# Kernel tuning notes

Measured on AMD Instinct MI355X. Metric: run time of the kernel, lower is better.

## Reference

```python
import jax, jax.numpy as jnp
import numpy as np

B, T, HID, H, Dk, Dv, K = 2, 1024, 1024, 8, 128, 128, 4
EPS = 1e-5


def _dwconv_causal(y, w, b):
    # y: [B,T,C], w: [C,1,K], b: [C]; torch Conv1d(padding=K-1) then [:, :, :T] == causal left-pad
    C = y.shape[-1]
    z = jnp.transpose(y, (0, 2, 1))  # [B,C,T]
    z = jax.lax.conv_general_dilated(
        z, w, window_strides=(1,), padding=[(K - 1, 0)],
        feature_group_count=C, dimension_numbers=("NCH", "OIH", "NCH"))
    z = z + b[None, :, None]
    return jnp.transpose(z, (0, 2, 1))


def _forward(x, Wq, Wk, Wv, conv_q_w, conv_q_b, conv_k_w, conv_k_b,
             conv_v_w, conv_v_b, Wa, ba, Wb, bb, Wg, Wo, ln_g, ln_b):
    b_, t_ = x.shape[0], x.shape[1]
    q = jax.nn.silu(_dwconv_causal(x @ Wq, conv_q_w, conv_q_b))
    k = jax.nn.silu(_dwconv_causal(x @ Wk, conv_k_w, conv_k_b))
    v = jax.nn.silu(_dwconv_causal(x @ Wv, conv_v_w, conv_v_b))
    q = q.reshape(b_, t_, H, Dk)
    k = k.reshape(b_, t_, H, Dk) * (Dk ** -0.5)
    v = v.reshape(b_, t_, H, Dv)
    alpha = jax.nn.sigmoid(x @ Wa + ba)  # [B,T,H]
    beta = jax.nn.sigmoid(x @ Wb + bb)   # [B,T,H]

    # time-major for scan
    qt = jnp.transpose(q, (1, 0, 2, 3))  # [T,B,H,Dk]
    kt = jnp.transpose(k, (1, 0, 2, 3))
    vt = jnp.transpose(v, (1, 0, 2, 3))  # [T,B,H,Dv]
    at = jnp.transpose(alpha, (1, 0, 2))  # [T,B,H]
    bt = jnp.transpose(beta, (1, 0, 2))

    def step(S, inp):
        q_t, k_t, v_t, a_t, b_t = inp
        sk = jnp.einsum('bhij,bhj->bhi', S, k_t)          # S @ k
        err = sk - v_t                                     # [B,H,Dv]
        S = a_t[:, :, None, None] * S - b_t[:, :, None, None] * (err[..., None] * k_t[:, :, None, :])
        o_t = jnp.einsum('bhij,bhj->bhi', S, q_t)          # S @ q (post-update)
        return S, o_t

    S0 = jnp.zeros((b_, H, Dv, Dk), x.dtype)
    _, o = jax.lax.scan(step, S0, (qt, kt, vt, at, bt))
    o = jnp.transpose(o, (1, 0, 2, 3))  # [B,T,H,Dv]

    # LayerNorm over Dv
    mu = jnp.mean(o, axis=-1, keepdims=True)
    var = jnp.mean((o - mu) ** 2, axis=-1, keepdims=True)
    o = (o - mu) * jax.lax.rsqrt(var + EPS) * ln_g + ln_b

    g = jax.nn.sigmoid(x @ Wg).reshape(b_, t_, H, Dv)
    o = (o * g).reshape(b_, t_, H * Dv)
    return o @ Wo


def setup_inputs() -> dict:
    key = jax.random.key(0)
    ks = jax.random.split(key, 18)
    s = 0.02

    def n(k, shape, scale=s):
        return jax.random.normal(k, shape, jnp.float32) * scale

    return {
        "x": jax.random.normal(ks[0], (B, T, HID), jnp.float32),
        "Wq": n(ks[1], (HID, H * Dk)),
        "Wk": n(ks[2], (HID, H * Dk)),
        "Wv": n(ks[3], (HID, H * Dv)),
        "conv_q_w": n(ks[4], (H * Dk, 1, K), 0.25),
        "conv_q_b": n(ks[5], (H * Dk,), 0.1),
        "conv_k_w": n(ks[6], (H * Dk, 1, K), 0.25),
        "conv_k_b": n(ks[7], (H * Dk,), 0.1),
        "conv_v_w": n(ks[8], (H * Dv, 1, K), 0.25),
        "conv_v_b": n(ks[9], (H * Dv,), 0.1),
        "Wa": n(ks[10], (HID, H)),
        "ba": n(ks[11], (H,), 0.1),
        "Wb": n(ks[12], (HID, H)),
        "bb": n(ks[13], (H,), 0.1),
        "Wg": n(ks[14], (HID, H * Dv)),
        "Wo": n(ks[15], (H * Dv, HID)),
        "ln_g": jnp.ones((Dv,), jnp.float32),
        "ln_b": jnp.zeros((Dv,), jnp.float32),
    }


def reference(x, Wq, Wk, Wv, conv_q_w, conv_q_b, conv_k_w, conv_k_b,
              conv_v_w, conv_v_b, Wa, ba, Wb, bb, Wg, Wo, ln_g, ln_b):
    return _forward(x, Wq, Wk, Wv, conv_q_w, conv_q_b, conv_k_w, conv_k_b,
                    conv_v_w, conv_v_b, Wa, ba, Wb, bb, Wg, Wo, ln_g, ln_b)
```

## Files before the change

kernel.cpp:

```cpp
#include <hip/hip_runtime.h>

#define TSEQ 1024
#define HID_ 1024
#define NH 8
#define DK 128
#define DV 128
#define ROWS 2048
#define SZf (ROWS * HID_)
#define LCH 64
#define NCK 16
#define KSTR 136
#define ESTR 65

typedef __attribute__((ext_vector_type(8))) short short8;
typedef __attribute__((ext_vector_type(4))) float f32x4;
#define MFMA __builtin_amdgcn_mfma_f32_16x16x32_bf16

__device__ __forceinline__ float sig_(float x) { return 1.f / (1.f + __expf(-x)); }

__device__ __forceinline__ ushort f2bf(float f) {
    unsigned int u = __builtin_bit_cast(unsigned int, f);
    u += 0x7FFF + ((u >> 16) & 1);
    return (ushort)(u >> 16);
}
__device__ __forceinline__ float bf2f(ushort u) {
    return __builtin_bit_cast(float, ((unsigned int)u) << 16);
}
__device__ __forceinline__ unsigned int pk2(float lo, float hi) {
    return (unsigned int)f2bf(lo) | ((unsigned int)f2bf(hi) << 16);
}

__device__ __forceinline__ void gload16(const void* g, void* l) {
    __builtin_amdgcn_global_load_lds(
        (const __attribute__((address_space(1))) unsigned int*)g,
        (__attribute__((address_space(3))) unsigned int*)l, 16, 0, 0);
}

__global__ __launch_bounds__(256)
void k_x2bf(const float* __restrict__ x, ushort* __restrict__ xb)
{
    const size_t i8 = (size_t)blockIdx.x * 256 + threadIdx.x;
    float4 v0 = *(const float4*)(x + i8 * 8);
    float4 v1 = *(const float4*)(x + i8 * 8 + 4);
    uint4 o;
    o.x = pk2(v0.x, v0.y); o.y = pk2(v0.z, v0.w);
    o.z = pk2(v1.x, v1.y); o.w = pk2(v1.z, v1.w);
    *(uint4*)(xb + i8 * 8) = o;
}

__global__ __launch_bounds__(256)
void k_wT(const float* __restrict__ s0, const float* __restrict__ s1,
          const float* __restrict__ s2, const float* __restrict__ s3,
          ushort* __restrict__ dst)
{
    const int z = blockIdx.z;
    const float* W = (z == 0) ? s0 : (z == 1) ? s1 : (z == 2) ? s2 : s3;
    ushort* WT = dst + (size_t)z * (1024 * 1024);
    __shared__ float t[64][65];
    const int n0 = blockIdx.x * 64, k0 = blockIdx.y * 64;
    const int rr = threadIdx.x >> 4, cc = threadIdx.x & 15;
#pragma unroll
    for (int i = 0; i < 4; ++i) {
        const int row = i * 16 + rr;
        float4 v = *(const float4*)(W + (size_t)(k0 + row) * 1024 + n0 + cc * 4);
        t[row][cc * 4 + 0] = v.x; t[row][cc * 4 + 1] = v.y;
        t[row][cc * 4 + 2] = v.z; t[row][cc * 4 + 3] = v.w;
    }
    __syncthreads();
#pragma unroll
    for (int i = 0; i < 4; ++i) {
        const int n = i * 16 + rr;
        const int kc = cc * 4;
        ushort4 o;
        o.x = f2bf(t[kc + 0][n]); o.y = f2bf(t[kc + 1][n]);
        o.z = f2bf(t[kc + 2][n]); o.w = f2bf(t[kc + 3][n]);
        *(ushort4*)(WT + (size_t)(n0 + n) * 1024 + k0 + kc) = o;
    }
}

__device__ __forceinline__ void gemm_tile_mfma(const ushort* __restrict__ A,
                                               const ushort* __restrict__ BT,
                                               float* __restrict__ C,
                                               int brow, int bcol)
{
    __shared__ ushort As[128 * 64];
    __shared__ ushort Bs[128 * 64];
    const int tid  = threadIdx.x;
    const int lane = tid & 63;
    const int wv   = tid >> 6;
    const int wm   = (wv >> 1) * 64;
    const int wn   = (wv & 1) * 64;
    const int l15  = lane & 15;
    const int lq   = lane >> 4;

    f32x4 acc[4][4];
#pragma unroll
    for (int i = 0; i < 4; ++i)
#pragma unroll
        for (int j = 0; j < 4; ++j)
#pragma unroll
            for (int e = 0; e < 4; ++e) acc[i][j][e] = 0.f;

    for (int k0 = 0; k0 < 1024; k0 += 64) {
        __syncthreads();
#pragma unroll
        for (int j = 0; j < 4; ++j) {
            const int idx  = j * 256 + tid;
            const int row  = idx >> 3;
            const int gcol = ((idx & 7) ^ (row & 7)) * 8;
            const int ldst = (j * 256 + wv * 64) * 8;
            gload16(A  + (size_t)(brow + row) * 1024 + k0 + gcol, As + ldst);
            gload16(BT + (size_t)(bcol + row) * 1024 + k0 + gcol, Bs + ldst);
        }
        __syncthreads();
#pragma unroll
        for (int kk = 0; kk < 2; ++kk) {
            short8 af[4], bf[4];
#pragma unroll
            for (int i = 0; i < 4; ++i) {
                const int ra = wm + i * 16 + l15;
                af[i] = *(const short8*)(As + ra * 64 + (((kk * 4 + lq) ^ (ra & 7)) * 8));
            }
#pragma unroll
            for (int j = 0; j < 4; ++j) {
                const int rb = wn + j * 16 + l15;
                bf[j] = *(const short8*)(Bs + rb * 64 + (((kk * 4 + lq) ^ (rb & 7)) * 8));
            }
#pragma unroll
            for (int i = 0; i < 4; ++i)
#pragma unroll
                for (int j = 0; j < 4; ++j)
                    acc[i][j] = MFMA(af[i], bf[j], acc[i][j], 0, 0, 0);
        }
    }
    const int l4 = lane >> 4;
#pragma unroll
    for (int i = 0; i < 4; ++i)
#pragma unroll
        for (int j = 0; j < 4; ++j)
#pragma unroll
            for (int r = 0; r < 4; ++r)
                C[(size_t)(brow + wm + i * 16 + l4 * 4 + r) * 1024 +
                  bcol + wn + j * 16 + l15] = acc[i][j][r];
}

__global__ __launch_bounds__(256)
void k_gemm4(const ushort* __restrict__ A, const ushort* __restrict__ WT,
             float* __restrict__ Cbase)
{
    const ushort* BT = WT + (size_t)blockIdx.z * (1024 * 1024);
    float* C = Cbase + (size_t)blockIdx.z * SZf;
    gemm_tile_mfma(A, BT, C, blockIdx.y * 128, blockIdx.x * 128);
}

__global__ __launch_bounds__(256)
void k_gemm1(const ushort* __restrict__ A, const ushort* __restrict__ BT,
             float* __restrict__ C)
{
    gemm_tile_mfma(A, BT, C, blockIdx.y * 128, blockIdx.x * 128);
}

__global__ __launch_bounds__(256)
void k_ab(const float* __restrict__ x, const float* __restrict__ Wa,
          const float* __restrict__ ba, const float* __restrict__ Wb,
          const float* __restrict__ bb, float* __restrict__ aT,
          float* __restrict__ bT)
{
    const int r = blockIdx.x * 4 + (threadIdx.x >> 6);
    const int lane = threadIdx.x & 63;
    const int b = r >> 10, t = r & 1023;
    const float* xr = x + (size_t)r * HID_;
    float acc[16];
#pragma unroll
    for (int n = 0; n < 16; ++n) acc[n] = 0.f;
    for (int c = lane; c < HID_; c += 64) {
        const float xv = xr[c];
        const float* wa = Wa + c * 8;
        const float* wb = Wb + c * 8;
#pragma unroll
        for (int n = 0; n < 8; ++n) {
            acc[n]     = fmaf(xv, wa[n], acc[n]);
            acc[8 + n] = fmaf(xv, wb[n], acc[8 + n]);
        }
    }
#pragma unroll
    for (int n = 0; n < 16; ++n) {
#pragma unroll
        for (int m = 32; m; m >>= 1) acc[n] += __shfl_xor(acc[n], m);
    }
    if (lane < 8) {
        aT[(size_t)(b * 8 + lane) * TSEQ + t] = sig_(acc[lane] + ba[lane]);
        bT[(size_t)(b * 8 + lane) * TSEQ + t] = sig_(acc[8 + lane] + bb[lane]);
    }
}

__global__ __launch_bounds__(256)
void k_conv(const float* __restrict__ qf, const float* __restrict__ kf,
            const float* __restrict__ vf,
            const float* __restrict__ wq, const float* __restrict__ bq,
            const float* __restrict__ wk, const float* __restrict__ bk,
            const float* __restrict__ wv, const float* __restrict__ bv,
            ushort* __restrict__ Qst, ushort* __restrict__ Kst,
            ushort* __restrict__ Vrm)
{
    const int j = blockIdx.x >> 1, cg = blockIdx.x & 1;
    const int b = blockIdx.y, z = blockIdx.z;
    const float* src  = (z == 0) ? qf : (z == 1) ? kf : vf;
    const float* w    = (z == 0) ? wq : (z == 1) ? wk : wv;
    const float* bias = (z == 0) ? bq : (z == 1) ? bk : bv;
    const float scale = (z == 1) ? 0.08838834764831845f : 1.f;
    const int c2 = cg * 512 + threadIdx.x * 2;
    const float w0a = w[c2 * 4],     w1a = w[c2 * 4 + 1], w2a = w[c2 * 4 + 2], w3a = w[c2 * 4 + 3];
    const float w0b = w[c2 * 4 + 4], w1b = w[c2 * 4 + 5], w2b = w[c2 * 4 + 6], w3b = w[c2 * 4 + 7];
    const float bsa = bias[c2], bsb = bias[c2 + 1];
    float ya0 = 0.f, ya1 = 0.f, ya2 = 0.f, yb0 = 0.f, yb1 = 0.f, yb2 = 0.f;
    if (j > 0) {
#pragma unroll
        for (int i = 0; i < 3; ++i) {
            float2 t = *(const float2*)(src + (size_t)(b * TSEQ + j * 64 - 3 + i) * HID_ + c2);
            if (i == 0) { ya0 = t.x; yb0 = t.y; }
            else if (i == 1) { ya1 = t.x; yb1 = t.y; }
            else { ya2 = t.x; yb2 = t.y; }
        }
    }
    const int h = c2 >> 7, dk = c2 & 127;
    const int cid = (b * 8 + h) * 16 + j;
    ushort* dst = (z == 0) ? Qst : Kst;
#pragma unroll 4
    for (int tl = 0; tl < 64; ++tl) {
        float2 xv = *(const float2*)(src + (size_t)(b * TSEQ + j * 64 + tl) * HID_ + c2);
        float a0 = fmaf(w0a, ya0, fmaf(w1a, ya1, fmaf(w2a, ya2, fmaf(w3a, xv.x, bsa))));
        float a1 = fmaf(w0b, yb0, fmaf(w1b, yb1, fmaf(w2b, yb2, fmaf(w3b, xv.y, bsb))));
        const float s0 = a0 * sig_(a0) * scale;
        const float s1 = a1 * sig_(a1) * scale;
        const uint p = pk2(s0, s1);
        if (z < 2) *(uint*)(dst + (size_t)cid * 8192 + tl * 128 + dk) = p;
        else       *(uint*)(Vrm + (size_t)(b * TSEQ + j * 64 + tl) * HID_ + c2) = p;
        ya0 = ya1; ya1 = ya2; ya2 = xv.x;
        yb0 = yb1; yb1 = yb2; yb2 = xv.y;
    }
}

__global__ __launch_bounds__(256)
void k_stageprep(const ushort* __restrict__ Kst, const ushort* __restrict__ Qst,
                 const ushort* __restrict__ Vrm,
                 const float* __restrict__ aT, const float* __restrict__ bT,
                 ushort* __restrict__ KTst, ushort* __restrict__ VstT,
                 ushort* __restrict__ Mg, ushort* __restrict__ Gg,
                 float* __restrict__ pug, float* __restrict__ pog,
                 float* __restrict__ dtotg)
{
    const int cid = blockIdx.x;
    const int bh = cid >> 4, c = cid & 15;
    const int b = bh >> 3, h = bh & 7;
    const int tid = threadIdx.x;
    const int t0 = c * LCH;

    __shared__ ushort Kb[64 * KSTR], Qb[64 * KSTR];
    __shared__ ushort Vl[128 * 72];
    __shared__ float Ef[64 * ESTR];
    __shared__ float Mf[64 * ESTR];
    __shared__ float cums[64], bv[64];

    if (tid < 64) {
        const float a = aT[(size_t)bh * TSEQ + t0 + tid];
        bv[tid] = bT[(size_t)bh * TSEQ + t0 + tid];
        float cs = __logf(a);
#pragma unroll
        for (int d = 1; d < 64; d <<= 1) {
            float pv = __shfl_up(cs, d);
            if (tid >= d) cs += pv;
        }
        cums[tid] = cs;
    }
    const size_t go = (size_t)cid * 8192;
#pragma unroll
    for (int j = 0; j < 4; ++j) {
        const int i16 = tid + j * 256;
        const int row = i16 >> 4, col = (i16 & 15) * 8;
        *(uint4*)(Kb + row * KSTR + col) = *(const uint4*)(Kst + go + i16 * 8);
        *(uint4*)(Qb + row * KSTR + col) = *(const uint4*)(Qst + go + i16 * 8);
    }
#pragma unroll
    for (int j = 0; j < 4; ++j) {
        const int i16 = tid + j * 256;
        const int row = i16 >> 4, c8 = (i16 & 15) * 8;
        ushort tmp[8];
        *(uint4*)tmp = *(const uint4*)(Vrm + (size_t)(b * TSEQ + t0 + row) * HID_ + h * DV + c8);
#pragma unroll
        for (int e = 0; e < 8; ++e)
            Vl[(c8 + e) * 72 + row] = tmp[e];
    }
    __syncthreads();

    const float ctop = cums[63];
#pragma unroll
    for (int j = 0; j < 4; ++j) {
        const int idx = tid + j * 256;
        const int dv = idx >> 3, tq = (idx & 7) * 8;
        *(uint4*)(VstT + go + dv * 64 + tq) = *(const uint4*)(Vl + dv * 72 + tq);
        const int dk = idx >> 3, tt = (idx & 7) * 8;
        ushort tmp[8];
#pragma unroll
        for (int e = 0; e < 8; ++e)
            tmp[e] = f2bf(bf2f(Kb[(tt + e) * KSTR + dk]) * __expf(ctop - cums[tt + e]));
        *(uint4*)(KTst + go + dk * 64 + tt) = *(uint4*)tmp;
    }

    const int wv = tid >> 6, l = tid & 63, l15 = l & 15, lq = l >> 4;
    const int k8o = lq * 8;
    f32x4 accK[4], accQ4[4];
#pragma unroll
    for (int j = 0; j < 4; ++j) {
        accK[j] = f32x4{0.f, 0.f, 0.f, 0.f};
        accQ4[j] = f32x4{0.f, 0.f, 0.f, 0.f};
    }
#pragma unroll
    for (int kk = 0; kk < 4; ++kk) {
        short8 aK = *(const short8*)(Kb + (wv * 16 + l15) * KSTR + kk * 32 + k8o);
        short8 aQ = *(const short8*)(Qb + (wv * 16 + l15) * KSTR + kk * 32 + k8o);
#pragma unroll
        for (int js = 0; js < 4; ++js) {
            short8 bK = *(const short8*)(Kb + (js * 16 + l15) * KSTR + kk * 32 + k8o);
            accK[js]  = MFMA(aK, bK, accK[js], 0, 0, 0);
            accQ4[js] = MFMA(aQ, bK, accQ4[js], 0, 0, 0);
        }
    }
    ushort* Gc = Gg + (size_t)cid * 4096;
#pragma unroll
    for (int js = 0; js < 4; ++js) {
#pragma unroll
        for (int r = 0; r < 4; ++r) {
            const int t = wv * 16 + lq * 4 + r;
            const int s = js * 16 + l15;
            const float cp = (t > 0) ? cums[t - 1] : 0.f;
            Ef[t * ESTR + s] = (s < t) ? __expf(cp - cums[s]) * accK[js][r] : 0.f;
            const float gv = (s <= t) ? __expf(cums[t] - cums[s]) * accQ4[js][r] : 0.f;
            Gc[t * 64 + s] = f2bf(gv);
        }
    }
    __syncthreads();

    if (tid < 64) {
        const int s = tid;
        for (int r = 0; r < 64; ++r) Mf[r * ESTR + s] = 0.f;
        Mf[s * ESTR + s] = bv[s];
        for (int t = 1; t < 64; ++t) {
            float s0 = 0.f, s1 = 0.f;
            int r = 0;
            for (; r + 1 < t; r += 2) {
                s0 = fmaf(Ef[t * ESTR + r],     Mf[r * ESTR + s],       s0);
                s1 = fmaf(Ef[t * ESTR + r + 1], Mf[(r + 1) * ESTR + s], s1);
            }
            if (r < t) s0 = fmaf(Ef[t * ESTR + r], Mf[r * ESTR + s], s0);
            if (s < t) Mf[t * ESTR + s] = -bv[t] * (s0 + s1);
        }
    }
    __syncthreads();
    ushort* Mc = Mg + (size_t)cid * 4096;
#pragma unroll
    for (int j = 0; j < 16; ++j) {
        const int e = tid + j * 256;
        Mc[e] = f2bf(Mf[(e >> 6) * ESTR + (e & 63)]);
    }
    if (tid < 64) {
        const float cp = (tid > 0) ? cums[tid - 1] : 0.f;
        pug[cid * 64 + tid] = __expf(cp);
        pog[cid * 64 + tid] = __expf(cums[tid]);
        if (tid == 0) dtotg[cid] = __expf(cums[63]);
    }
}

__global__ __launch_bounds__(256)
void k_scan2(const ushort* __restrict__ Kst, const ushort* __restrict__ KTst,
             const ushort* __restrict__ VstT, const ushort* __restrict__ Mg,
             const float* __restrict__ pug, const float* __restrict__ dtg,
             ushort* __restrict__ Sst, ushort* __restrict__ Wst)
{
    const int blk = blockIdx.x;
    const int bh = blk >> 1, half = blk & 1;
    const int tid = threadIdx.x;
    const int wv = tid >> 6, l = tid & 63, l15 = l & 15, lq = l >> 4;
    const int k8o = lq * 8;
    const int dvw = wv * 16;

    __shared__ ushort Kb[64 * KSTR];
    __shared__ ushort KTb[128 * 72];
    __shared__ ushort Mb[64 * 72];
    __shared__ ushort Vb[64 * 72];
    __shared__ ushort Shb[64 * KSTR], Slb[64 * KSTR];
    __shared__ ushort Yb[64 * 72], Wb[64 * 72];
    __shared__ float puv[64], dts[1];

    f32x4 accS[8];
#pragma unroll
    for (int m = 0; m < 8; ++m) accS[m] = f32x4{0.f, 0.f, 0.f, 0.f};

    uint4 rk[4], rkt[4], rm[2], rv[2];
    float rpu = 0.f, rdt = 0.f;

    auto LOADC = [&](int cc) {
        const int cid = bh * 16 + cc;
        const size_t go = (size_t)cid * 8192;
#pragma unroll
        for (int j = 0; j < 4; ++j) {
            rk[j]  = *(const uint4*)(Kst  + go + (tid + j * 256) * 8);
            rkt[j] = *(const uint4*)(KTst + go + (tid + j * 256) * 8);
        }
#pragma unroll
        for (int j = 0; j < 2; ++j) {
            rm[j] = *(const uint4*)(Mg + (size_t)cid * 4096 + (tid + j * 256) * 8);
            rv[j] = *(const uint4*)(VstT + go + half * 4096 + (tid + j * 256) * 8);
        }
        if (tid < 64) {
            rpu = pug[cid * 64 + tid];
            if (tid == 0) rdt = dtg[cid];
        }
    };
    auto WRITEC = [&]() {
#pragma unroll
        for (int j = 0; j < 4; ++j) {
            const int i16 = tid + j * 256;
            *(uint4*)(Kb  + (i16 >> 4) * KSTR + (i16 & 15) * 8) = rk[j];
            *(uint4*)(KTb + (i16 >> 3) * 72   + (i16 & 7) * 8)  = rkt[j];
        }
#pragma unroll
        for (int j = 0; j < 2; ++j) {
            const int i8 = tid + j * 256;
            *(uint4*)(Mb + (i8 >> 3) * 72 + (i8 & 7) * 8) = rm[j];
            *(uint4*)(Vb + (i8 >> 3) * 72 + (i8 & 7) * 8) = rv[j];
        }
        if (tid < 64) {
            puv[tid] = rpu;
            if (tid == 0) dts[0] = rdt;
        }
    };

    LOADC(0); WRITEC();
    __syncthreads();

    for (int c = 0; c < NCK; ++c) {
        if (c + 1 < NCK) LOADC(c + 1);

#pragma unroll
        for (int m = 0; m < 8; ++m) {
            ushort h4[4], l4v[4];
#pragma unroll
            for (int r = 0; r < 4; ++r) {
                const float sv = accS[m][r];
                const ushort hi = f2bf(sv);
                h4[r] = hi;
                l4v[r] = f2bf(sv - bf2f(hi));
            }
            *(uint2*)(Shb + (dvw + l15) * KSTR + m * 16 + lq * 4) = *(uint2*)h4;
            *(uint2*)(Slb + (dvw + l15) * KSTR + m * 16 + lq * 4) = *(uint2*)l4v;
        }
        f32x4 accU[4];
#pragma unroll
        for (int jj = 0; jj < 4; ++jj) accU[jj] = f32x4{0.f, 0.f, 0.f, 0.f};
#pragma unroll
        for (int kk = 0; kk < 4; ++kk) {
            short8 sh = *(const short8*)(Shb + (dvw + l15) * KSTR + kk * 32 + k8o);
            short8 sl = *(const short8*)(Slb + (dvw + l15) * KSTR + kk * 32 + k8o);
#pragma unroll
            for (int jj = 0; jj < 4; ++jj) {
                short8 ka = *(const short8*)(Kb + (jj * 16 + l15) * KSTR + kk * 32 + k8o);
                accU[jj] = MFMA(ka, sh, accU[jj], 0, 0, 0);
                accU[jj] = MFMA(ka, sl, accU[jj], 0, 0, 0);
            }
        }
#pragma unroll
        for (int jj = 0; jj < 4; ++jj) {
            float pu4[4];
            *(float4*)pu4 = *(const float4*)(puv + jj * 16 + lq * 4);
            ushort v4[4];
            *(uint2*)v4 = *(const uint2*)(Vb + (dvw + l15) * 72 + jj * 16 + lq * 4);
            ushort y4[4];
#pragma unroll
            for (int r = 0; r < 4; ++r)
                y4[r] = f2bf(bf2f(v4[r]) - pu4[r] * accU[jj][r]);
            *(uint2*)(Yb + (dvw + l15) * 72 + jj * 16 + lq * 4) = *(uint2*)y4;
        }
        f32x4 accW[4];
#pragma unroll
        for (int jj = 0; jj < 4; ++jj) accW[jj] = f32x4{0.f, 0.f, 0.f, 0.f};
#pragma unroll
        for (int kk = 0; kk < 2; ++kk) {
            short8 yb = *(const short8*)(Yb + (dvw + l15) * 72 + kk * 32 + k8o);
#pragma unroll
            for (int jj = 0; jj < 4; ++jj) {
                short8 mf = *(const short8*)(Mb + (jj * 16 + l15) * 72 + kk * 32 + k8o);
                accW[jj] = MFMA(mf, yb, accW[jj], 0, 0, 0);
            }
        }
#pragma unroll
        for (int jj = 0; jj < 4; ++jj) {
            ushort w4[4];
#pragma unroll
            for (int r = 0; r < 4; ++r)
                w4[r] = f2bf(accW[jj][r]);
            *(uint2*)(Wb + (dvw + l15) * 72 + jj * 16 + lq * 4) = *(uint2*)w4;
        }
        const float dt = dts[0];
#pragma unroll
        for (int m = 0; m < 8; ++m)
#pragma unroll
            for (int r = 0; r < 4; ++r) accS[m][r] *= dt;
#pragma unroll
        for (int kk = 0; kk < 2; ++kk) {
            short8 wc = *(const short8*)(Wb + (dvw + l15) * 72 + kk * 32 + k8o);
#pragma unroll
            for (int m = 0; m < 8; ++m) {
                short8 kt = *(const short8*)(KTb + (m * 16 + l15) * 72 + kk * 32 + k8o);
                accS[m] = MFMA(kt, wc, accS[m], 0, 0, 0);
            }
        }
        {
            const int cid = bh * 16 + c;
#pragma unroll
            for (int j = 0; j < 4; ++j) {
                const int idx = l + j * 64;
                const int dvo = idx >> 4, ko = (idx & 15) * 8;
                *(uint4*)(Sst + (size_t)cid * 16384 +
                          (half * 64 + dvw + dvo) * 128 + ko) =
                    *(const uint4*)(Shb + (dvw + dvo) * KSTR + ko);
            }
#pragma unroll
            for (int j = 0; j < 2; ++j) {
                const int idx = l + j * 64;
                const int dvo = idx >> 3, t8 = (idx & 7) * 8;
                *(uint4*)(Wst + (size_t)cid * 8192 +
                          (half * 64 + dvw + dvo) * 64 + t8) =
                    *(const uint4*)(Wb + (dvw + dvo) * 72 + t8);
            }
        }
        __syncthreads();
        if (c + 1 < NCK) WRITEC();
        __syncthreads();
    }
}

__global__ __launch_bounds__(256)
void k_out(const ushort* __restrict__ Sst, const ushort* __restrict__ Qst,
           const ushort* __restrict__ Gg, const ushort* __restrict__ Wst,
           const float* __restrict__ pog, const float* __restrict__ g_lin,
           const float* __restrict__ lng, const float* __restrict__ lnb,
           ushort* __restrict__ ogb)
{
    const int cid = blockIdx.x;
    const int bh = cid >> 4, c = cid & 15;
    const int b = bh >> 3, h = bh & 7;
    const int t0 = c * LCH;
    const int tid = threadIdx.x;
    const int wv = tid >> 6, l = tid & 63, l15 = l & 15, lq = l >> 4;
    const int k8o = lq * 8;

    __shared__ ushort Sb[128 * KSTR];
    __shared__ ushort Qb[64 * KSTR];
    __shared__ ushort Gb[64 * 72];
    __shared__ ushort Wqb[128 * 72];
    __shared__ float  Ot[64 * 132];
    __shared__ float  pov[64];

#pragma unroll
    for (int j = 0; j < 8; ++j) {
        const int i16 = tid + j * 256;
        *(uint4*)(Sb + (i16 >> 4) * KSTR + (i16 & 15) * 8) =
            *(const uint4*)(Sst + (size_t)cid * 16384 + i16 * 8);
    }
#pragma unroll
    for (int j = 0; j < 4; ++j) {
        const int i16 = tid + j * 256;
        *(uint4*)(Qb + (i16 >> 4) * KSTR + (i16 & 15) * 8) =
            *(const uint4*)(Qst + (size_t)cid * 8192 + i16 * 8);
        const int i8 = i16;
        *(uint4*)(Wqb + (i8 >> 3) * 72 + (i8 & 7) * 8) =
            *(const uint4*)(Wst + (size_t)cid * 8192 + i8 * 8);
    }
#pragma unroll
    for (int j = 0; j < 2; ++j) {
        const int i8 = tid + j * 256;
        *(uint4*)(Gb + (i8 >> 3) * 72 + (i8 & 7) * 8) =
            *(const uint4*)(Gg + (size_t)cid * 4096 + i8 * 8);
    }
    if (tid < 64) pov[tid] = pog[cid * 64 + tid];
    __syncthreads();

#pragma unroll
    for (int i = 0; i < 2; ++i) {
        const int dvt = wv * 2 + i;
        f32x4 acc[4], acg[4];
#pragma unroll
        for (int jj = 0; jj < 4; ++jj) {
            acc[jj] = f32x4{0.f, 0.f, 0.f, 0.f};
            acg[jj] = f32x4{0.f, 0.f, 0.f, 0.f};
        }
#pragma unroll
        for (int kk = 0; kk < 4; ++kk) {
            short8 sa = *(const short8*)(Sb + (dvt * 16 + l15) * KSTR + kk * 32 + k8o);
#pragma unroll
            for (int jj = 0; jj < 4; ++jj) {
                short8 qb = *(const short8*)(Qb + (jj * 16 + l15) * KSTR + kk * 32 + k8o);
                acc[jj] = MFMA(sa, qb, acc[jj], 0, 0, 0);
            }
        }
#pragma unroll
        for (int kk = 0; kk < 2; ++kk) {
            short8 wa = *(const short8*)(Wqb + (dvt * 16 + l15) * 72 + kk * 32 + k8o);
#pragma unroll
            for (int jj = 0; jj < 4; ++jj) {
                short8 gb = *(const short8*)(Gb + (jj * 16 + l15) * 72 + kk * 32 + k8o);
                acg[jj] = MFMA(wa, gb, acg[jj], 0, 0, 0);
            }
        }
#pragma unroll
        for (int jj = 0; jj < 4; ++jj) {
            const int t = jj * 16 + l15;
            const float po = pov[t];
            float4 o4;
            o4.x = po * acc[jj][0] + acg[jj][0];
            o4.y = po * acc[jj][1] + acg[jj][1];
            o4.z = po * acc[jj][2] + acg[jj][2];
            o4.w = po * acc[jj][3] + acg[jj][3];
            *(float4*)(Ot + t * 132 + dvt * 16 + lq * 4) = o4;
        }
    }
    __syncthreads();

    const int d = l * 2;
    const float lg0 = lng[d], lg1 = lng[d + 1];
    const float lb0 = lnb[d], lb1 = lnb[d + 1];
    const size_t btbase = (size_t)b * TSEQ + t0 + wv * 16;
#pragma unroll 1
    for (int rr = 0; rr < 16; ++rr) {
        const int t = wv * 16 + rr;
        float2 xv = *(const float2*)(Ot + t * 132 + d);
        float s = xv.x + xv.y;
#pragma unroll
        for (int m = 32; m; m >>= 1) s += __shfl_xor(s, m);
        const float mu = s * (1.f / 128.f);
        const float d0 = xv.x - mu, d1 = xv.y - mu;
        float v = d0 * d0 + d1 * d1;
#pragma unroll
        for (int m = 32; m; m >>= 1) v += __shfl_xor(v, m);
        const float inv = rsqrtf(v * (1.f / 128.f) + 1e-5f);
        const float* gp = g_lin + (btbase + rr) * HID_ + h * DV;
        const float g0 = sig_(gp[d]), g1 = sig_(gp[d + 1]);
        const float y0 = (d0 * inv * lg0 + lb0) * g0;
        const float y1 = (d1 * inv * lg1 + lb1) * g1;
        *(uint*)(ogb + (btbase + rr) * HID_ + h * DV + d) = pk2(y0, y1);
    }
}

extern "C" void kernel_launch(void* const* d_in, const int* in_sizes, int n_in,
                              void* d_out, int out_size, void* d_ws, size_t ws_size,
                              hipStream_t stream)
{
    const float* x   = (const float*)d_in[0];
    const float* Wq  = (const float*)d_in[1];
    const float* Wk  = (const float*)d_in[2];
    const float* Wv  = (const float*)d_in[3];
    const float* cqw = (const float*)d_in[4];
    const float* cqb = (const float*)d_in[5];
    const float* ckw = (const float*)d_in[6];
    const float* ckb = (const float*)d_in[7];
    const float* cvw = (const float*)d_in[8];
    const float* cvb = (const float*)d_in[9];
    const float* Wa  = (const float*)d_in[10];
    const float* ba  = (const float*)d_in[11];
    const float* Wb  = (const float*)d_in[12];
    const float* bb  = (const float*)d_in[13];
    const float* Wg  = (const float*)d_in[14];
    const float* Wo  = (const float*)d_in[15];
    const float* lng = (const float*)d_in[16];
    const float* lnb = (const float*)d_in[17];
    float* out = (float*)d_out;
    float* ws  = (float*)d_ws;

    float* q_lin = ws;
    float* k_lin = ws + 1 * (size_t)SZf;
    float* v_lin = ws + 2 * (size_t)SZf;
    float* g_lin = ws + 3 * (size_t)SZf;
    float* o_buf = ws + 4 * (size_t)SZf;
    float* aT    = ws + 5 * (size_t)SZf;
    float* bT    = aT + 16 * TSEQ;
    float* pug   = bT + 16 * TSEQ;
    float* pog   = pug + 256 * 64;
    float* dtg   = pog + 256 * 64;

    float*  tail = ws + 5 * (size_t)SZf + 131072;
    ushort* Kst  = (ushort*)tail;
    ushort* Qst  = Kst + (size_t)256 * 8192;
    ushort* xbf  = Qst + (size_t)256 * 8192;
    ushort* Vrm  = xbf;
    ushort* KTst = xbf + (size_t)256 * 8192;

    ushort* WT4  = (ushort*)o_buf;
    ushort* WoT  = (ushort*)k_lin;
    ushort* ogb  = (ushort*)q_lin;
    ushort* VstT = (ushort*)q_lin + (size_t)2 * 1024 * 1024;
    ushort* Sst  = (ushort*)o_buf;
    ushort* Mg   = (ushort*)out;
    ushort* Gg   = Mg + (size_t)256 * 4096;
    ushort* Wst  = Gg + (size_t)256 * 4096;

    k_x2bf<<<1024, 256, 0, stream>>>(x, xbf);
    k_wT<<<dim3(16, 16, 4), 256, 0, stream>>>(Wq, Wk, Wv, Wg, WT4);
    k_gemm4<<<dim3(8, 16, 4), 256, 0, stream>>>(xbf, WT4, ws);
    k_ab<<<512, 256, 0, stream>>>(x, Wa, ba, Wb, bb, aT, bT);
    k_conv<<<dim3(32, 2, 3), 256, 0, stream>>>(q_lin, k_lin, v_lin,
                                               cqw, cqb, ckw, ckb, cvw, cvb,
                                               Qst, Kst, Vrm);
    k_wT<<<dim3(16, 16, 1), 256, 0, stream>>>(Wo, Wo, Wo, Wo, WoT);
    k_stageprep<<<256, 256, 0, stream>>>(Kst, Qst, Vrm, aT, bT,
                                         KTst, VstT, Mg, Gg, pug, pog, dtg);
    k_scan2<<<32, 256, 0, stream>>>(Kst, KTst, VstT, Mg, pug, dtg, Sst, Wst);
    k_out<<<256, 256, 0, stream>>>(Sst, Qst, Gg, Wst, pog, g_lin, lng, lnb, ogb);
    k_gemm1<<<dim3(8, 16), 256, 0, stream>>>(ogb, WoT, out);
}
```

Baseline: 217.7 us.

## Fuse conv into stage prep, emit bf16 projections, double-buffer scan chunks

The QKVG projection GEMM now writes bf16 instead of fp32, which halves its output traffic. The causal depthwise conv + SiLU is folded into the per-chunk stage-prep kernel, so conv results go straight into shared memory instead of round-tripping through global memory. The Wo transpose is merged into the main weight-transpose launch, and the scan kernel double-buffers its chunk operands in LDS to drop one barrier per iteration. In exchange, the stored projections and the gate input lose precision, and shared-memory use in the scan kernel grows.

```diff
diff --git a/kernel.cpp b/kernel.cpp
--- a/kernel.cpp
+++ b/kernel.cpp
@@ -10,6 +10,7 @@
 #define LCH 64
 #define NCK 16
 #define KSTR 136
+#define KS2 132
 #define ESTR 65
 
 typedef __attribute__((ext_vector_type(8))) short short8;
@@ -51,11 +52,13 @@
 __global__ __launch_bounds__(256)
 void k_wT(const float* __restrict__ s0, const float* __restrict__ s1,
           const float* __restrict__ s2, const float* __restrict__ s3,
-          ushort* __restrict__ dst)
+          const float* __restrict__ s4,
+          ushort* __restrict__ dst, ushort* __restrict__ dstWo)
 {
     const int z = blockIdx.z;
-    const float* W = (z == 0) ? s0 : (z == 1) ? s1 : (z == 2) ? s2 : s3;
-    ushort* WT = dst + (size_t)z * (1024 * 1024);
+    const float* W = (z == 0) ? s0 : (z == 1) ? s1 : (z == 2) ? s2
+                   : (z == 3) ? s3 : s4;
+    ushort* WT = (z < 4) ? dst + (size_t)z * (1024 * 1024) : dstWo;
     __shared__ float t[64][65];
     const int n0 = blockIdx.x * 64, k0 = blockIdx.y * 64;
     const int rr = threadIdx.x >> 4, cc = threadIdx.x & 15;
@@ -78,9 +81,10 @@
     }
 }
 
+template<typename CT>
 __device__ __forceinline__ void gemm_tile_mfma(const ushort* __restrict__ A,
                                                const ushort* __restrict__ BT,
-                                               float* __restrict__ C,
+                                               CT* __restrict__ C,
                                                int brow, int bcol)
 {
     __shared__ ushort As[128 * 64];
@@ -139,25 +143,28 @@
 #pragma unroll
         for (int j = 0; j < 4; ++j)
 #pragma unroll
-            for (int r = 0; r < 4; ++r)
-                C[(size_t)(brow + wm + i * 16 + l4 * 4 + r) * 1024 +
-                  bcol + wn + j * 16 + l15] = acc[i][j][r];
+            for (int r = 0; r < 4; ++r) {
+                const size_t o = (size_t)(brow + wm + i * 16 + l4 * 4 + r) * 1024 +
+                                 bcol + wn + j * 16 + l15;
+                if constexpr (sizeof(CT) == 2) C[o] = f2bf(acc[i][j][r]);
+                else                           C[o] = acc[i][j][r];
+            }
 }
 
 __global__ __launch_bounds__(256)
 void k_gemm4(const ushort* __restrict__ A, const ushort* __restrict__ WT,
-             float* __restrict__ Cbase)
+             ushort* __restrict__ Cbase)
 {
     const ushort* BT = WT + (size_t)blockIdx.z * (1024 * 1024);
-    float* C = Cbase + (size_t)blockIdx.z * SZf;
-    gemm_tile_mfma(A, BT, C, blockIdx.y * 128, blockIdx.x * 128);
+    ushort* C = Cbase + (size_t)blockIdx.z * SZf;
+    gemm_tile_mfma<ushort>(A, BT, C, blockIdx.y * 128, blockIdx.x * 128);
 }
 
 __global__ __launch_bounds__(256)
 void k_gemm1(const ushort* __restrict__ A, const ushort* __restrict__ BT,
              float* __restrict__ C)
 {
-    gemm_tile_mfma(A, BT, C, blockIdx.y * 128, blockIdx.x * 128);
+    gemm_tile_mfma<float>(A, BT, C, blockIdx.y * 128, blockIdx.x * 128);
 }
 
 __global__ __launch_bounds__(256)
@@ -195,108 +202,95 @@
 }
 
 __global__ __launch_bounds__(256)
-void k_conv(const float* __restrict__ qf, const float* __restrict__ kf,
-            const float* __restrict__ vf,
-            const float* __restrict__ wq, const float* __restrict__ bq,
-            const float* __restrict__ wk, const float* __restrict__ bk,
-            const float* __restrict__ wv, const float* __restrict__ bv,
-            ushort* __restrict__ Qst, ushort* __restrict__ Kst,
-            ushort* __restrict__ Vrm)
-{
-    const int j = blockIdx.x >> 1, cg = blockIdx.x & 1;
-    const int b = blockIdx.y, z = blockIdx.z;
-    const float* src  = (z == 0) ? qf : (z == 1) ? kf : vf;
-    const float* w    = (z == 0) ? wq : (z == 1) ? wk : wv;
-    const float* bias = (z == 0) ? bq : (z == 1) ? bk : bv;
-    const float scale = (z == 1) ? 0.08838834764831845f : 1.f;
-    const int c2 = cg * 512 + threadIdx.x * 2;
-    const float w0a = w[c2 * 4],     w1a = w[c2 * 4 + 1], w2a = w[c2 * 4 + 2], w3a = w[c2 * 4 + 3];
-    const float w0b = w[c2 * 4 + 4], w1b = w[c2 * 4 + 5], w2b = w[c2 * 4 + 6], w3b = w[c2 * 4 + 7];
-    const float bsa = bias[c2], bsb = bias[c2 + 1];
-    float ya0 = 0.f, ya1 = 0.f, ya2 = 0.f, yb0 = 0.f, yb1 = 0.f, yb2 = 0.f;
-    if (j > 0) {
-#pragma unroll
-        for (int i = 0; i < 3; ++i) {
-            float2 t = *(const float2*)(src + (size_t)(b * TSEQ + j * 64 - 3 + i) * HID_ + c2);
-            if (i == 0) { ya0 = t.x; yb0 = t.y; }
-            else if (i == 1) { ya1 = t.x; yb1 = t.y; }
-            else { ya2 = t.x; yb2 = t.y; }
-        }
-    }
-    const int h = c2 >> 7, dk = c2 & 127;
-    const int cid = (b * 8 + h) * 16 + j;
-    ushort* dst = (z == 0) ? Qst : Kst;
-#pragma unroll 4
-    for (int tl = 0; tl < 64; ++tl) {
-        float2 xv = *(const float2*)(src + (size_t)(b * TSEQ + j * 64 + tl) * HID_ + c2);
-        float a0 = fmaf(w0a, ya0, fmaf(w1a, ya1, fmaf(w2a, ya2, fmaf(w3a, xv.x, bsa))));
-        float a1 = fmaf(w0b, yb0, fmaf(w1b, yb1, fmaf(w2b, yb2, fmaf(w3b, xv.y, bsb))));
-        const float s0 = a0 * sig_(a0) * scale;
-        const float s1 = a1 * sig_(a1) * scale;
-        const uint p = pk2(s0, s1);
-        if (z < 2) *(uint*)(dst + (size_t)cid * 8192 + tl * 128 + dk) = p;
-        else       *(uint*)(Vrm + (size_t)(b * TSEQ + j * 64 + tl) * HID_ + c2) = p;
-        ya0 = ya1; ya1 = ya2; ya2 = xv.x;
-        yb0 = yb1; yb1 = yb2; yb2 = xv.y;
-    }
-}
-
-__global__ __launch_bounds__(256)
-void k_stageprep(const ushort* __restrict__ Kst, const ushort* __restrict__ Qst,
-                 const ushort* __restrict__ Vrm,
-                 const float* __restrict__ aT, const float* __restrict__ bT,
-                 ushort* __restrict__ KTst, ushort* __restrict__ VstT,
-                 ushort* __restrict__ Mg, ushort* __restrict__ Gg,
-                 float* __restrict__ pug, float* __restrict__ pog,
-                 float* __restrict__ dtotg)
+void k_convprep(const ushort* __restrict__ qb_, const ushort* __restrict__ kb_,
+                const ushort* __restrict__ vb_,
+                const float* __restrict__ wq, const float* __restrict__ bq,
+                const float* __restrict__ wk, const float* __restrict__ bk,
+                const float* __restrict__ wv, const float* __restrict__ bv,
+                const float* __restrict__ aT, const float* __restrict__ bT,
+                ushort* __restrict__ Kst, ushort* __restrict__ Qst,
+                ushort* __restrict__ VstT, ushort* __restrict__ KTst,
+                ushort* __restrict__ Mg, ushort* __restrict__ Gg,
+                float* __restrict__ pug, float* __restrict__ pog,
+                float* __restrict__ dtotg)
 {
     const int cid = blockIdx.x;
-    const int bh = cid >> 4, c = cid & 15;
+    const int bh = cid >> 4, j = cid & 15;
     const int b = bh >> 3, h = bh & 7;
     const int tid = threadIdx.x;
-    const int t0 = c * LCH;
+    const int t0 = j * LCH;
 
     __shared__ ushort Kb[64 * KSTR], Qb[64 * KSTR];
     __shared__ ushort Vl[128 * 72];
     __shared__ float Ef[64 * ESTR];
     __shared__ float Mf[64 * ESTR];
-    __shared__ float cums[64], bv[64];
-
-    if (tid < 64) {
-        const float a = aT[(size_t)bh * TSEQ + t0 + tid];
-        bv[tid] = bT[(size_t)bh * TSEQ + t0 + tid];
+    __shared__ float cums[64], bv2[64];
+
+    if (tid >= 192) {
+        const int lane = tid - 192;
+        const float a = aT[(size_t)bh * TSEQ + t0 + lane];
+        bv2[lane] = bT[(size_t)bh * TSEQ + t0 + lane];
         float cs = __logf(a);
 #pragma unroll
         for (int d = 1; d < 64; d <<= 1) {
             float pv = __shfl_up(cs, d);
-            if (tid >= d) cs += pv;
-        }
-        cums[tid] = cs;
-    }
+            if (lane >= d) cs += pv;
+        }
+        cums[lane] = cs;
+    } else {
+        const int z = tid >> 6;
+        const int c2 = (tid & 63) * 2;
+        const ushort* src  = (z == 0) ? qb_ : (z == 1) ? kb_ : vb_;
+        const float* w     = (z == 0) ? wq : (z == 1) ? wk : wv;
+        const float* bias  = (z == 0) ? bq : (z == 1) ? bk : bv;
+        const float scale  = (z == 1) ? 0.08838834764831845f : 1.f;
+        const int gc = h * 128 + c2;
+        const float w0a = w[gc * 4],     w1a = w[gc * 4 + 1], w2a = w[gc * 4 + 2], w3a = w[gc * 4 + 3];
+        const float w0b = w[gc * 4 + 4], w1b = w[gc * 4 + 5], w2b = w[gc * 4 + 6], w3b = w[gc * 4 + 7];
+        const float bsa = bias[gc], bsb = bias[gc + 1];
+        float ya0 = 0.f, ya1 = 0.f, ya2 = 0.f, yb0 = 0.f, yb1 = 0.f, yb2 = 0.f;
+        if (j > 0) {
+#pragma unroll
+            for (int i = 0; i < 3; ++i) {
+                uint u = *(const uint*)(src + (size_t)(b * TSEQ + t0 - 3 + i) * HID_ + gc);
+                const float lo = bf2f((ushort)u), hi = bf2f((ushort)(u >> 16));
+                if (i == 0) { ya0 = lo; yb0 = hi; }
+                else if (i == 1) { ya1 = lo; yb1 = hi; }
+                else { ya2 = lo; yb2 = hi; }
+            }
+        }
+#pragma unroll 4
+        for (int tl = 0; tl < 64; ++tl) {
+            uint u = *(const uint*)(src + (size_t)(b * TSEQ + t0 + tl) * HID_ + gc);
+            const float x0 = bf2f((ushort)u), x1 = bf2f((ushort)(u >> 16));
+            float a0 = fmaf(w0a, ya0, fmaf(w1a, ya1, fmaf(w2a, ya2, fmaf(w3a, x0, bsa))));
+            float a1 = fmaf(w0b, yb0, fmaf(w1b, yb1, fmaf(w2b, yb2, fmaf(w3b, x1, bsb))));
+            const float s0 = a0 * sig_(a0) * scale;
+            const float s1 = a1 * sig_(a1) * scale;
+            if (z == 0)      *(uint*)(Qb + tl * KSTR + c2) = pk2(s0, s1);
+            else if (z == 1) *(uint*)(Kb + tl * KSTR + c2) = pk2(s0, s1);
+            else {
+                Vl[(c2 + 0) * 72 + tl] = f2bf(s0);
+                Vl[(c2 + 1) * 72 + tl] = f2bf(s1);
+            }
+            ya0 = ya1; ya1 = ya2; ya2 = x0;
+            yb0 = yb1; yb1 = yb2; yb2 = x1;
+        }
+    }
+    __syncthreads();
+
     const size_t go = (size_t)cid * 8192;
-#pragma unroll
-    for (int j = 0; j < 4; ++j) {
-        const int i16 = tid + j * 256;
+    const float ctop = cums[63];
+#pragma unroll
+    for (int jx = 0; jx < 4; ++jx) {
+        const int i16 = tid + jx * 256;
         const int row = i16 >> 4, col = (i16 & 15) * 8;
-        *(uint4*)(Kb + row * KSTR + col) = *(const uint4*)(Kst + go + i16 * 8);
-        *(uint4*)(Qb + row * KSTR + col) = *(const uint4*)(Qst + go + i16 * 8);
-    }
-#pragma unroll
-    for (int j = 0; j < 4; ++j) {
-        const int i16 = tid + j * 256;
-        const int row = i16 >> 4, c8 = (i16 & 15) * 8;
-        ushort tmp[8];
-        *(uint4*)tmp = *(const uint4*)(Vrm + (size_t)(b * TSEQ + t0 + row) * HID_ + h * DV + c8);
-#pragma unroll
-        for (int e = 0; e < 8; ++e)
-            Vl[(c8 + e) * 72 + row] = tmp[e];
-    }
-    __syncthreads();
-
-    const float ctop = cums[63];
-#pragma unroll
-    for (int j = 0; j < 4; ++j) {
-        const int idx = tid + j * 256;
+        *(uint4*)(Kst + go + i16 * 8) = *(const uint4*)(Kb + row * KSTR + col);
+        *(uint4*)(Qst + go + i16 * 8) = *(const uint4*)(Qb + row * KSTR + col);
+    }
+#pragma unroll
+    for (int jx = 0; jx < 4; ++jx) {
+        const int idx = tid + jx * 256;
         const int dv = idx >> 3, tq = (idx & 7) * 8;
         *(uint4*)(VstT + go + dv * 64 + tq) = *(const uint4*)(Vl + dv * 72 + tq);
         const int dk = idx >> 3, tt = (idx & 7) * 8;
@@ -307,18 +301,18 @@
         *(uint4*)(KTst + go + dk * 64 + tt) = *(uint4*)tmp;
     }
 
-    const int wv = tid >> 6, l = tid & 63, l15 = l & 15, lq = l >> 4;
+    const int wv2 = tid >> 6, l = tid & 63, l15 = l & 15, lq = l >> 4;
     const int k8o = lq * 8;
     f32x4 accK[4], accQ4[4];
 #pragma unroll
-    for (int j = 0; j < 4; ++j) {
-        accK[j] = f32x4{0.f, 0.f, 0.f, 0.f};
-        accQ4[j] = f32x4{0.f, 0.f, 0.f, 0.f};
+    for (int jx = 0; jx < 4; ++jx) {
+        accK[jx] = f32x4{0.f, 0.f, 0.f, 0.f};
+        accQ4[jx] = f32x4{0.f, 0.f, 0.f, 0.f};
     }
 #pragma unroll
     for (int kk = 0; kk < 4; ++kk) {
-        short8 aK = *(const short8*)(Kb + (wv * 16 + l15) * KSTR + kk * 32 + k8o);
-        short8 aQ = *(const short8*)(Qb + (wv * 16 + l15) * KSTR + kk * 32 + k8o);
+        short8 aK = *(const short8*)(Kb + (wv2 * 16 + l15) * KSTR + kk * 32 + k8o);
+        short8 aQ = *(const short8*)(Qb + (wv2 * 16 + l15) * KSTR + kk * 32 + k8o);
 #pragma unroll
         for (int js = 0; js < 4; ++js) {
             short8 bK = *(const short8*)(Kb + (js * 16 + l15) * KSTR + kk * 32 + k8o);
@@ -331,7 +325,7 @@
     for (int js = 0; js < 4; ++js) {
 #pragma unroll
         for (int r = 0; r < 4; ++r) {
-            const int t = wv * 16 + lq * 4 + r;
+            const int t = wv2 * 16 + lq * 4 + r;
             const int s = js * 16 + l15;
             const float cp = (t > 0) ? cums[t - 1] : 0.f;
             Ef[t * ESTR + s] = (s < t) ? __expf(cp - cums[s]) * accK[js][r] : 0.f;
@@ -344,7 +338,7 @@
     if (tid < 64) {
         const int s = tid;
         for (int r = 0; r < 64; ++r) Mf[r * ESTR + s] = 0.f;
-        Mf[s * ESTR + s] = bv[s];
+        Mf[s * ESTR + s] = bv2[s];
         for (int t = 1; t < 64; ++t) {
             float s0 = 0.f, s1 = 0.f;
             int r = 0;
@@ -353,14 +347,14 @@
                 s1 = fmaf(Ef[t * ESTR + r + 1], Mf[(r + 1) * ESTR + s], s1);
             }
             if (r < t) s0 = fmaf(Ef[t * ESTR + r], Mf[r * ESTR + s], s0);
-            if (s < t) Mf[t * ESTR + s] = -bv[t] * (s0 + s1);
+            if (s < t) Mf[t * ESTR + s] = -bv2[t] * (s0 + s1);
         }
     }
     __syncthreads();
     ushort* Mc = Mg + (size_t)cid * 4096;
 #pragma unroll
-    for (int j = 0; j < 16; ++j) {
-        const int e = tid + j * 256;
+    for (int jx = 0; jx < 16; ++jx) {
+        const int e = tid + jx * 256;
         Mc[e] = f2bf(Mf[(e >> 6) * ESTR + (e & 63)]);
     }
     if (tid < 64) {
@@ -384,13 +378,14 @@
     const int k8o = lq * 8;
     const int dvw = wv * 16;
 
-    __shared__ ushort Kb[64 * KSTR];
-    __shared__ ushort KTb[128 * 72];
-    __shared__ ushort Mb[64 * 72];
-    __shared__ ushort Vb[64 * 72];
-    __shared__ ushort Shb[64 * KSTR], Slb[64 * KSTR];
+    __shared__ ushort Kdb[2][64 * KS2];
+    __shared__ ushort KTdb[2][128 * 72];
+    __shared__ ushort Mdb[2][64 * 72];
+    __shared__ ushort Vdb[2][64 * 72];
+    __shared__ ushort Shb[64 * KS2], Slb[64 * KS2];
     __shared__ ushort Yb[64 * 72], Wb[64 * 72];
-    __shared__ float puv[64], dts[1];
+    __shared__ float puv[2][64];
+    __shared__ float dts[2];
 
     f32x4 accS[8];
 #pragma unroll
@@ -403,44 +398,51 @@
         const int cid = bh * 16 + cc;
         const size_t go = (size_t)cid * 8192;
 #pragma unroll
-        for (int j = 0; j < 4; ++j) {
-            rk[j]  = *(const uint4*)(Kst  + go + (tid + j * 256) * 8);
-            rkt[j] = *(const uint4*)(KTst + go + (tid + j * 256) * 8);
-        }
-#pragma unroll
-        for (int j = 0; j < 2; ++j) {
-            rm[j] = *(const uint4*)(Mg + (size_t)cid * 4096 + (tid + j * 256) * 8);
-            rv[j] = *(const uint4*)(VstT + go + half * 4096 + (tid + j * 256) * 8);
+        for (int jx = 0; jx < 4; ++jx) {
+            rk[jx]  = *(const uint4*)(Kst  + go + (tid + jx * 256) * 8);
+            rkt[jx] = *(const uint4*)(KTst + go + (tid + jx * 256) * 8);
+        }
+#pragma unroll
+        for (int jx = 0; jx < 2; ++jx) {
+            rm[jx] = *(const uint4*)(Mg + (size_t)cid * 4096 + (tid + jx * 256) * 8);
+            rv[jx] = *(const uint4*)(VstT + go + half * 4096 + (tid + jx * 256) * 8);
         }
         if (tid < 64) {
             rpu = pug[cid * 64 + tid];
             if (tid == 0) rdt = dtg[cid];
         }
     };
-    auto WRITEC = [&]() {
-#pragma unroll
-        for (int j = 0; j < 4; ++j) {
-            const int i16 = tid + j * 256;
-            *(uint4*)(Kb  + (i16 >> 4) * KSTR + (i16 & 15) * 8) = rk[j];
-            *(uint4*)(KTb + (i16 >> 3) * 72   + (i16 & 7) * 8)  = rkt[j];
-        }
-#pragma unroll
-        for (int j = 0; j < 2; ++j) {
-            const int i8 = tid + j * 256;
-            *(uint4*)(Mb + (i8 >> 3) * 72 + (i8 & 7) * 8) = rm[j];
-            *(uint4*)(Vb + (i8 >> 3) * 72 + (i8 & 7) * 8) = rv[j];
+    auto WRITEC = [&](int buf) {
+#pragma unroll
+        for (int jx = 0; jx < 4; ++jx) {
+            const int i16 = tid + jx * 256;
+            *(uint4*)(&Kdb[buf][(i16 >> 4) * KS2 + (i16 & 15) * 8]) = rk[jx];
+            *(uint4*)(&KTdb[buf][(i16 >> 3) * 72 + (i16 & 7) * 8])  = rkt[jx];
+        }
+#pragma unroll
+        for (int jx = 0; jx < 2; ++jx) {
+            const int i8 = tid + jx * 256;
+            *(uint4*)(&Mdb[buf][(i8 >> 3) * 72 + (i8 & 7) * 8]) = rm[jx];
+            *(uint4*)(&Vdb[buf][(i8 >> 3) * 72 + (i8 & 7) * 8]) = rv[jx];
         }
         if (tid < 64) {
-            puv[tid] = rpu;
-            if (tid == 0) dts[0] = rdt;
+            puv[buf][tid] = rpu;
+            if (tid == 0) dts[buf] = rdt;
         }
     };
 
-    LOADC(0); WRITEC();
+    LOADC(0); WRITEC(0);
     __syncthreads();
 
     for (int c = 0; c < NCK; ++c) {
+        const int cur = c & 1;
         if (c + 1 < NCK) LOADC(c + 1);
+        const ushort* Kb = Kdb[cur];
+        const ushort* KTb = KTdb[cur];
+        const ushort* Mb = Mdb[cur];
+        const ushort* Vb = Vdb[cur];
+        const float* pv2 = puv[cur];
+        const float dt = dts[cur];
 
 #pragma unroll
         for (int m = 0; m < 8; ++m) {
@@ -452,19 +454,19 @@
                 h4[r] = hi;
                 l4v[r] = f2bf(sv - bf2f(hi));
             }
-            *(uint2*)(Shb + (dvw + l15) * KSTR + m * 16 + lq * 4) = *(uint2*)h4;
-            *(uint2*)(Slb + (dvw + l15) * KSTR + m * 16 + lq * 4) = *(uint2*)l4v;
+            *(uint2*)(Shb + (dvw + l15) * KS2 + m * 16 + lq * 4) = *(uint2*)h4;
+            *(uint2*)(Slb + (dvw + l15) * KS2 + m * 16 + lq * 4) = *(uint2*)l4v;
         }
         f32x4 accU[4];
 #pragma unroll
         for (int jj = 0; jj < 4; ++jj) accU[jj] = f32x4{0.f, 0.f, 0.f, 0.f};
 #pragma unroll
         for (int kk = 0; kk < 4; ++kk) {
-            short8 sh = *(const short8*)(Shb + (dvw + l15) * KSTR + kk * 32 + k8o);
-            short8 sl = *(const short8*)(Slb + (dvw + l15) * KSTR + kk * 32 + k8o);
+            short8 sh = *(const short8*)(Shb + (dvw + l15) * KS2 + kk * 32 + k8o);
+            short8 sl = *(const short8*)(Slb + (dvw + l15) * KS2 + kk * 32 + k8o);
 #pragma unroll
             for (int jj = 0; jj < 4; ++jj) {
-                short8 ka = *(const short8*)(Kb + (jj * 16 + l15) * KSTR + kk * 32 + k8o);
+                short8 ka = *(const short8*)(Kb + (jj * 16 + l15) * KS2 + kk * 32 + k8o);
                 accU[jj] = MFMA(ka, sh, accU[jj], 0, 0, 0);
                 accU[jj] = MFMA(ka, sl, accU[jj], 0, 0, 0);
             }
@@ -472,7 +474,7 @@
 #pragma unroll
         for (int jj = 0; jj < 4; ++jj) {
             float pu4[4];
-            *(float4*)pu4 = *(const float4*)(puv + jj * 16 + lq * 4);
+            *(float4*)pu4 = *(const float4*)(pv2 + jj * 16 + lq * 4);
             ushort v4[4];
             *(uint2*)v4 = *(const uint2*)(Vb + (dvw + l15) * 72 + jj * 16 + lq * 4);
             ushort y4[4];
@@ -501,7 +503,6 @@
                 w4[r] = f2bf(accW[jj][r]);
             *(uint2*)(Wb + (dvw + l15) * 72 + jj * 16 + lq * 4) = *(uint2*)w4;
         }
-        const float dt = dts[0];
 #pragma unroll
         for (int m = 0; m < 8; ++m)
 #pragma unroll
@@ -518,24 +519,23 @@
         {
             const int cid = bh * 16 + c;
 #pragma unroll
-            for (int j = 0; j < 4; ++j) {
-                const int idx = l + j * 64;
+            for (int jx = 0; jx < 4; ++jx) {
+                const int idx = l + jx * 64;
                 const int dvo = idx >> 4, ko = (idx & 15) * 8;
                 *(uint4*)(Sst + (size_t)cid * 16384 +
                           (half * 64 + dvw + dvo) * 128 + ko) =
-                    *(const uint4*)(Shb + (dvw + dvo) * KSTR + ko);
-            }
-#pragma unroll
-            for (int j = 0; j < 2; ++j) {
-                const int idx = l + j * 64;
+                    *(const uint4*)(Shb + (dvw + dvo) * KS2 + ko);
+            }
+#pragma unroll
+            for (int jx = 0; jx < 2; ++jx) {
+                const int idx = l + jx * 64;
                 const int dvo = idx >> 3, t8 = (idx & 7) * 8;
                 *(uint4*)(Wst + (size_t)cid * 8192 +
                           (half * 64 + dvw + dvo) * 64 + t8) =
                     *(const uint4*)(Wb + (dvw + dvo) * 72 + t8);
             }
         }
-        __syncthreads();
-        if (c + 1 < NCK) WRITEC();
+        if (c + 1 < NCK) WRITEC(cur ^ 1);
         __syncthreads();
     }
 }
@@ -543,7 +543,7 @@
 __global__ __launch_bounds__(256)
 void k_out(const ushort* __restrict__ Sst, const ushort* __restrict__ Qst,
            const ushort* __restrict__ Gg, const ushort* __restrict__ Wst,
-           const float* __restrict__ pog, const float* __restrict__ g_lin,
+           const float* __restrict__ pog, const ushort* __restrict__ gb_,
            const float* __restrict__ lng, const float* __restrict__ lnb,
            ushort* __restrict__ ogb)
 {
@@ -563,23 +563,22 @@
     __shared__ float  pov[64];
 
 #pragma unroll
-    for (int j = 0; j < 8; ++j) {
-        const int i16 = tid + j * 256;
+    for (int jx = 0; jx < 8; ++jx) {
+        const int i16 = tid + jx * 256;
         *(uint4*)(Sb + (i16 >> 4) * KSTR + (i16 & 15) * 8) =
             *(const uint4*)(Sst + (size_t)cid * 16384 + i16 * 8);
     }
 #pragma unroll
-    for (int j = 0; j < 4; ++j) {
-        const int i16 = tid + j * 256;
+    for (int jx = 0; jx < 4; ++jx) {
+        const int i16 = tid + jx * 256;
         *(uint4*)(Qb + (i16 >> 4) * KSTR + (i16 & 15) * 8) =
             *(const uint4*)(Qst + (size_t)cid * 8192 + i16 * 8);
-        const int i8 = i16;
-        *(uint4*)(Wqb + (i8 >> 3) * 72 + (i8 & 7) * 8) =
-            *(const uint4*)(Wst + (size_t)cid * 8192 + i8 * 8);
-    }
-#pragma unroll
-    for (int j = 0; j < 2; ++j) {
-        const int i8 = tid + j * 256;
+        *(uint4*)(Wqb + (i16 >> 3) * 72 + (i16 & 7) * 8) =
+            *(const uint4*)(Wst + (size_t)cid * 8192 + i16 * 8);
+    }
+#pragma unroll
+    for (int jx = 0; jx < 2; ++jx) {
+        const int i8 = tid + jx * 256;
         *(uint4*)(Gb + (i8 >> 3) * 72 + (i8 & 7) * 8) =
             *(const uint4*)(Gg + (size_t)cid * 4096 + i8 * 8);
     }
@@ -644,8 +643,8 @@
 #pragma unroll
         for (int m = 32; m; m >>= 1) v += __shfl_xor(v, m);
         const float inv = rsqrtf(v * (1.f / 128.f) + 1e-5f);
-        const float* gp = g_lin + (btbase + rr) * HID_ + h * DV;
-        const float g0 = sig_(gp[d]), g1 = sig_(gp[d + 1]);
+        const uint gu = *(const uint*)(gb_ + (btbase + rr) * HID_ + h * DV + d);
+        const float g0 = sig_(bf2f((ushort)gu)), g1 = sig_(bf2f((ushort)(gu >> 16)));
         const float y0 = (d0 * inv * lg0 + lb0) * g0;
         const float y1 = (d1 * inv * lg1 + lb1) * g1;
         *(uint*)(ogb + (btbase + rr) * HID_ + h * DV + d) = pk2(y0, y1);
@@ -677,44 +676,42 @@
     float* out = (float*)d_out;
     float* ws  = (float*)d_ws;
 
-    float* q_lin = ws;
-    float* k_lin = ws + 1 * (size_t)SZf;
-    float* v_lin = ws + 2 * (size_t)SZf;
-    float* g_lin = ws + 3 * (size_t)SZf;
-    float* o_buf = ws + 4 * (size_t)SZf;
-    float* aT    = ws + 5 * (size_t)SZf;
-    float* bT    = aT + 16 * TSEQ;
-    float* pug   = bT + 16 * TSEQ;
-    float* pog   = pug + 256 * 64;
-    float* dtg   = pog + 256 * 64;
+    ushort* qb_ = (ushort*)ws;
+    ushort* kb_ = qb_ + (size_t)SZf;
+    ushort* vb_ = qb_ + (size_t)2 * SZf;
+    ushort* gb_ = qb_ + (size_t)3 * SZf;
+
+    ushort* ogb  = (ushort*)(ws + 2 * (size_t)SZf);
+    ushort* VstT = ogb + (size_t)2 * 1024 * 1024;
+    ushort* WoT  = (ushort*)(ws + 3 * (size_t)SZf);
+    float*  o_buf = ws + 4 * (size_t)SZf;
+    ushort* WT4  = (ushort*)o_buf;
+    ushort* Sst  = (ushort*)o_buf;
+    float* aT  = ws + 5 * (size_t)SZf;
+    float* bT  = aT + 16 * TSEQ;
+    float* pug = bT + 16 * TSEQ;
+    float* pog = pug + 256 * 64;
+    float* dtg = pog + 256 * 64;
 
     float*  tail = ws + 5 * (size_t)SZf + 131072;
     ushort* Kst  = (ushort*)tail;
     ushort* Qst  = Kst + (size_t)256 * 8192;
     ushort* xbf  = Qst + (size_t)256 * 8192;
-    ushort* Vrm  = xbf;
-    ushort* KTst = xbf + (size_t)256 * 8192;
-
-    ushort* WT4  = (ushort*)o_buf;
-    ushort* WoT  = (ushort*)k_lin;
-    ushort* ogb  = (ushort*)q_lin;
-    ushort* VstT = (ushort*)q_lin + (size_t)2 * 1024 * 1024;
-    ushort* Sst  = (ushort*)o_buf;
-    ushort* Mg   = (ushort*)out;
-    ushort* Gg   = Mg + (size_t)256 * 4096;
-    ushort* Wst  = Gg + (size_t)256 * 4096;
+    ushort* KTst = xbf;
+
+    ushort* Mg  = (ushort*)out;
+    ushort* Gg  = Mg + (size_t)256 * 4096;
+    ushort* Wst = Gg + (size_t)256 * 4096;
 
     k_x2bf<<<1024, 256, 0, stream>>>(x, xbf);
-    k_wT<<<dim3(16, 16, 4), 256, 0, stream>>>(Wq, Wk, Wv, Wg, WT4);
-    k_gemm4<<<dim3(8, 16, 4), 256, 0, stream>>>(xbf, WT4, ws);
+    k_wT<<<dim3(16, 16, 5), 256, 0, stream>>>(Wq, Wk, Wv, Wg, Wo, WT4, WoT);
+    k_gemm4<<<dim3(8, 16, 4), 256, 0, stream>>>(xbf, WT4, qb_);
     k_ab<<<512, 256, 0, stream>>>(x, Wa, ba, Wb, bb, aT, bT);
-    k_conv<<<dim3(32, 2, 3), 256, 0, stream>>>(q_lin, k_lin, v_lin,
-                                               cqw, cqb, ckw, ckb, cvw, cvb,
-                                               Qst, Kst, Vrm);
-    k_wT<<<dim3(16, 16, 1), 256, 0, stream>>>(Wo, Wo, Wo, Wo, WoT);
-    k_stageprep<<<256, 256, 0, stream>>>(Kst, Qst, Vrm, aT, bT,
-                                         KTst, VstT, Mg, Gg, pug, pog, dtg);
+    k_convprep<<<256, 256, 0, stream>>>(qb_, kb_, vb_,
+                                        cqw, cqb, ckw, ckb, cvw, cvb,
+                                        aT, bT, Kst, Qst, VstT, KTst,
+                                        Mg, Gg, pug, pog, dtg);
     k_scan2<<<32, 256, 0, stream>>>(Kst, KTst, VstT, Mg, pug, dtg, Sst, Wst);
-    k_out<<<256, 256, 0, stream>>>(Sst, Qst, Gg, Wst, pog, g_lin, lng, lnb, ogb);
+    k_out<<<256, 256, 0, stream>>>(Sst, Qst, Gg, Wst, pog, gb_, lng, lnb, ogb);
     k_gemm1<<<dim3(8, 16), 256, 0, stream>>>(ogb, WoT, out);
 }
```

New measurement: 256.6 us (median of 3 runs). +17.9%, slower.
